# Performance work log

Measured on AMD Instinct MI355X. Metric: run time of the kernel, lower is better.

## Reference

```python
import jax, jax.numpy as jnp
import numpy as np

ATTN_SIZE = 64
ENC_SIZE = 512
HIDDEN_SIZE = 512
L, B = 2048, 64


def setup_inputs() -> dict:
    key = jax.random.key(0)
    k1, k2, k3, k4, k5, k6 = jax.random.split(key, 6)
    enc_outputs = jax.random.normal(k1, (L, B, ENC_SIZE), dtype=jnp.float32)
    lens = jax.random.randint(k2, (B,), 1, L + 1, dtype=jnp.int32)
    hidden_states = jax.random.normal(k3, (B, HIDDEN_SIZE), dtype=jnp.float32)
    # Xavier-normal params as in reset_params()
    W_enc = jax.random.normal(k4, (ENC_SIZE, ATTN_SIZE), dtype=jnp.float32) * np.sqrt(2.0 / (ENC_SIZE + ATTN_SIZE))
    W_hidden = jax.random.normal(k5, (HIDDEN_SIZE, ATTN_SIZE), dtype=jnp.float32) * np.sqrt(2.0 / (HIDDEN_SIZE + ATTN_SIZE))
    b_attn = jnp.zeros((ATTN_SIZE,), dtype=jnp.float32)
    v = jax.random.normal(k6, (ATTN_SIZE,), dtype=jnp.float32)
    return {"enc_outputs": enc_outputs, "lens": lens, "hidden_states": hidden_states,
            "W_enc": W_enc, "b_attn": b_attn, "W_hidden": W_hidden, "v": v}


def reference(enc_outputs, lens, hidden_states, W_enc, b_attn, W_hidden, v):
    l = enc_outputs.shape[0]
    # parts: (l, b, attn_size) — projection of encoder outputs
    parts = jnp.einsum('lbd,da->lba', enc_outputs, W_enc) + b_attn
    # additive (Bahdanau) score: tanh(parts + h @ W_hidden) . v -> (l, b)
    hid = hidden_states @ W_hidden  # (b, attn_size)
    scores = jnp.sum(jnp.tanh(parts + hid[None, :, :]) * v, axis=2)
    # faithful mask: 1.0 at valid positions, -inf at padding (original adds 1, a
    # constant shift that softmax cancels, but we reproduce the exact math)
    valid = jnp.arange(l, dtype=lens.dtype)[:, None] < lens[None, :]  # (l, b)
    mask = jnp.where(valid, jnp.float32(1.0), -jnp.inf)
    w = jax.nn.softmax(scores + mask, axis=0)  # softmax over sequence dim
    # weighted sum over sequence: (b, d)
    return jnp.einsum('lb,lbd->bd', w, enc_outputs)
```

## Files before the change

kernel.cpp:

```cpp
#include <hip/hip_runtime.h>
#include <math.h>

#define L_DIM 2048
#define B_DIM 64
#define D_DIM 512
#define A_DIM 64

__global__ void hb_kernel(const float* __restrict__ hidden,
                          const float* __restrict__ Wh,
                          const float* __restrict__ battn,
                          float* __restrict__ hb) {
    const int b = blockIdx.x;
    const int a = threadIdx.x;
    const float* hrow = hidden + b * D_DIM;
    float acc = battn[a];
#pragma unroll 8
    for (int d = 0; d < D_DIM; ++d) {
        acc += hrow[d] * Wh[d * A_DIM + a];
    }
    hb[b * A_DIM + a] = acc;
}

__global__ __launch_bounds__(256) void scores_kernel(
    const float* __restrict__ enc, const float* __restrict__ We,
    const float* __restrict__ hb, const float* __restrict__ v,
    const int* __restrict__ lens, float* __restrict__ scores) {
    const int l = blockIdx.x;
    const int tid = threadIdx.x;
    const int ty = tid >> 4;
    const int tx = tid & 15;

    __shared__ float As[32][68];
    __shared__ float Bs[32][68];
    __shared__ float red[64][17];

    float acc[4][4] = {};

    float4 areg[2], breg[2];

    const float* encl = enc + (size_t)l * B_DIM * D_DIM;

    auto loadTiles = [&](int k0) {
#pragma unroll
        for (int i = 0; i < 2; ++i) {
            const int c = tid + 256 * i;
            const int bb = c >> 3, kq = c & 7;
            areg[i] = *(const float4*)(encl + bb * D_DIM + k0 + kq * 4);
            const int kk = c >> 4, a4 = (c & 15) * 4;
            breg[i] = *(const float4*)(We + (k0 + kk) * A_DIM + a4);
        }
    };
    auto storeTiles = [&]() {
#pragma unroll
        for (int i = 0; i < 2; ++i) {
            const int c = tid + 256 * i;
            const int bb = c >> 3, kq = c & 7;
            As[kq * 4 + 0][bb] = areg[i].x;
            As[kq * 4 + 1][bb] = areg[i].y;
            As[kq * 4 + 2][bb] = areg[i].z;
            As[kq * 4 + 3][bb] = areg[i].w;
            const int kk = c >> 4, a4 = (c & 15) * 4;
            *(float4*)&Bs[kk][a4] = breg[i];
        }
    };

    loadTiles(0);
#pragma unroll 1
    for (int t = 0; t < 16; ++t) {
        __syncthreads();
        storeTiles();
        __syncthreads();
        if (t < 15) loadTiles((t + 1) * 32);
#pragma unroll
        for (int k = 0; k < 32; ++k) {
            const float4 av = *(const float4*)&As[k][ty * 4];
            const float4 bv = *(const float4*)&Bs[k][tx * 4];
            acc[0][0] += av.x * bv.x; acc[0][1] += av.x * bv.y;
            acc[0][2] += av.x * bv.z; acc[0][3] += av.x * bv.w;
            acc[1][0] += av.y * bv.x; acc[1][1] += av.y * bv.y;
            acc[1][2] += av.y * bv.z; acc[1][3] += av.y * bv.w;
            acc[2][0] += av.z * bv.x; acc[2][1] += av.z * bv.y;
            acc[2][2] += av.z * bv.z; acc[2][3] += av.z * bv.w;
            acc[3][0] += av.w * bv.x; acc[3][1] += av.w * bv.y;
            acc[3][2] += av.w * bv.z; acc[3][3] += av.w * bv.w;
        }
    }

    const float4 vv = *(const float4*)(v + tx * 4);
#pragma unroll
    for (int i = 0; i < 4; ++i) {
        const int bb = ty * 4 + i;
        const float4 hbv = *(const float4*)(hb + bb * A_DIM + tx * 4);
        float s = tanhf(acc[i][0] + hbv.x) * vv.x;
        s += tanhf(acc[i][1] + hbv.y) * vv.y;
        s += tanhf(acc[i][2] + hbv.z) * vv.z;
        s += tanhf(acc[i][3] + hbv.w) * vv.w;
        red[bb][tx] = s;
    }
    __syncthreads();
    if (tid < B_DIM) {
        const int bb = tid;
        float s = 0.f;
#pragma unroll
        for (int j = 0; j < 16; ++j) s += red[bb][j];
        s = (l < lens[bb]) ? (s + 1.0f) : -INFINITY;
        scores[(size_t)bb * L_DIM + l] = s;
    }
}

__global__ __launch_bounds__(256) void softmax_kernel(float* __restrict__ scores) {
    const int b = blockIdx.x;
    const int tid = threadIdx.x;
    float* s = scores + (size_t)b * L_DIM;
    __shared__ float red[256];

    float m = -INFINITY;
    for (int l = tid; l < L_DIM; l += 256) m = fmaxf(m, s[l]);
    red[tid] = m;
    __syncthreads();
    for (int off = 128; off > 0; off >>= 1) {
        if (tid < off) red[tid] = fmaxf(red[tid], red[tid + off]);
        __syncthreads();
    }
    m = red[0];
    __syncthreads();

    float z = 0.f;
    for (int l = tid; l < L_DIM; l += 256) z += expf(s[l] - m);
    red[tid] = z;
    __syncthreads();
    for (int off = 128; off > 0; off >>= 1) {
        if (tid < off) red[tid] += red[tid + off];
        __syncthreads();
    }
    const float inv = 1.0f / red[0];

    for (int l = tid; l < L_DIM; l += 256) s[l] = expf(s[l] - m) * inv;
}

__global__ __launch_bounds__(256) void zero_out_kernel(float* __restrict__ out) {
    out[blockIdx.x * 256 + threadIdx.x] = 0.f;
}

__global__ __launch_bounds__(128) void wsum_kernel(
    const float* __restrict__ enc, const float* __restrict__ w,
    float* __restrict__ out) {
    const int b = blockIdx.x;
    const int lc = blockIdx.y;
    const int tid = threadIdx.x;
    const int l0 = lc * (L_DIM / 16);

    float4 acc = {0.f, 0.f, 0.f, 0.f};
#pragma unroll 4
    for (int l = l0; l < l0 + (L_DIM / 16); ++l) {
        const float wt = w[(size_t)b * L_DIM + l];
        const float4 e =
            *(const float4*)(enc + ((size_t)l * B_DIM + b) * D_DIM + tid * 4);
        acc.x += wt * e.x; acc.y += wt * e.y;
        acc.z += wt * e.z; acc.w += wt * e.w;
    }
    float* o = out + (size_t)b * D_DIM + tid * 4;
    atomicAdd(o + 0, acc.x);
    atomicAdd(o + 1, acc.y);
    atomicAdd(o + 2, acc.z);
    atomicAdd(o + 3, acc.w);
}

extern "C" void kernel_launch(void* const* d_in, const int* in_sizes, int n_in,
                              void* d_out, int out_size, void* d_ws, size_t ws_size,
                              hipStream_t stream) {
    const float* enc    = (const float*)d_in[0];
    const int*   lens   = (const int*)d_in[1];
    const float* hidden = (const float*)d_in[2];
    const float* We     = (const float*)d_in[3];
    const float* battn  = (const float*)d_in[4];
    const float* Wh     = (const float*)d_in[5];
    const float* v      = (const float*)d_in[6];
    float* out = (float*)d_out;

    float* hb     = (float*)d_ws;
    float* scores = hb + B_DIM * A_DIM;

    hb_kernel<<<B_DIM, A_DIM, 0, stream>>>(hidden, Wh, battn, hb);
    scores_kernel<<<L_DIM, 256, 0, stream>>>(enc, We, hb, v, lens, scores);
    softmax_kernel<<<B_DIM, 256, 0, stream>>>(scores);
    zero_out_kernel<<<(B_DIM * D_DIM) / 256, 256, 0, stream>>>(out);
    wsum_kernel<<<dim3(B_DIM, 16), 128, 0, stream>>>(enc, scores, out);
}
```

Baseline: 516.1 us.

## Fuse scores, online softmax and weighted sum with split-bf16 MFMA

Adds a fused kernel that processes 64-position chunks per batch element. Each chunk of encoder data is loaded once, split into bf16 hi/lo parts in shared memory, and projected with bf16 MFMA using three products to keep near-fp32 accuracy. The kernel then computes a chunk-local online softmax and accumulates the weighted sum from the same staged data. A combine kernel merges the per-chunk partials. This removes the second full read of the encoder tensor, the separate softmax pass and the atomics. It costs extra MFMA work and conversion, and it only runs when the workspace is large enough; otherwise the old path is used.

New measurement: 509.1 us. About the same (-1.4%).

```diff
diff --git a/kernel.cpp b/kernel.cpp
--- a/kernel.cpp
+++ b/kernel.cpp
@@ -1,10 +1,31 @@
 #include <hip/hip_runtime.h>
+#include <hip/hip_bf16.h>
 #include <math.h>
 
 #define L_DIM 2048
 #define B_DIM 64
 #define D_DIM 512
 #define A_DIM 64
+
+#define CHUNK_L 64
+#define SUB_L 32
+#define N_CHUNK (L_DIM / CHUNK_L)
+#define EPAD 520
+
+typedef __attribute__((ext_vector_type(8))) short bf16x8;
+typedef __attribute__((ext_vector_type(4))) float f32x4;
+
+__device__ __forceinline__ void split_bf16(float x, short& hi, short& lo) {
+    __hip_bfloat16 h = __float2bfloat16(x);
+    float hf = __bfloat162float(h);
+    __hip_bfloat16 l = __float2bfloat16(x - hf);
+    hi = *reinterpret_cast<short*>(&h);
+    lo = *reinterpret_cast<short*>(&l);
+}
+__device__ __forceinline__ float bf16s_to_f(short s) {
+    unsigned int u = ((unsigned int)(unsigned short)s) << 16;
+    return __uint_as_float(u);
+}
 
 __global__ void hb_kernel(const float* __restrict__ hidden,
                           const float* __restrict__ Wh,
@@ -15,10 +36,231 @@
     const float* hrow = hidden + b * D_DIM;
     float acc = battn[a];
 #pragma unroll 8
-    for (int d = 0; d < D_DIM; ++d) {
-        acc += hrow[d] * Wh[d * A_DIM + a];
-    }
+    for (int d = 0; d < D_DIM; ++d) acc += hrow[d] * Wh[d * A_DIM + a];
     hb[b * A_DIM + a] = acc;
+}
+
+__global__ __launch_bounds__(256) void wt_kernel(const float* __restrict__ We,
+                                                 short* __restrict__ wt_hi,
+                                                 short* __restrict__ wt_lo) {
+    const int idx = blockIdx.x * 256 + threadIdx.x;
+    const int a = idx & 63;
+    const int d = idx >> 6;
+    float x = We[d * A_DIM + a];
+    short h, l;
+    split_bf16(x, h, l);
+    wt_hi[a * D_DIM + d] = h;
+    wt_lo[a * D_DIM + d] = l;
+}
+
+__global__ __launch_bounds__(256) void fused_kernel(
+    const float* __restrict__ enc, const short* __restrict__ wt_hi,
+    const short* __restrict__ wt_lo, const float* __restrict__ hb,
+    const float* __restrict__ v, const int* __restrict__ lens,
+    float* __restrict__ Om, float* __restrict__ mz) {
+    const int c = blockIdx.x;
+    const int b = blockIdx.y;
+    const int tid = threadIdx.x;
+    const int wave = tid >> 6;
+    const int lane = tid & 63;
+    const int quad = lane >> 4;
+    const int l15 = lane & 15;
+
+    __shared__ short Ehi[SUB_L][EPAD];
+    __shared__ short Elo[SUB_L][EPAD];
+    __shared__ float sred[SUB_L][2];
+    __shared__ float wl[SUB_L];
+    __shared__ float red[4][D_DIM];
+    __shared__ float msc[2];
+
+    const int len_b = lens[b];
+
+    const int lt = wave >> 1;
+    const int ah = wave & 1;
+    const int a0 = (2 * ah) * 16 + l15;
+    const int a1 = a0 + 16;
+
+    const float hb0 = hb[b * A_DIM + a0];
+    const float hb1 = hb[b * A_DIM + a1];
+    const float v0 = v[a0];
+    const float v1 = v[a1];
+
+    float Oacc[8];
+#pragma unroll
+    for (int i = 0; i < 8; ++i) Oacc[i] = 0.f;
+    float mA = -INFINITY, ZA = 0.f;
+
+    const int g = tid >> 6;
+    const int d0 = (tid & 63) * 8;
+
+#pragma unroll 1
+    for (int sub = 0; sub < 2; ++sub) {
+        const int l_base = c * CHUNK_L + sub * SUB_L;
+
+        __syncthreads();
+
+        {
+            const float* src = enc + ((size_t)l_base * B_DIM + b) * D_DIM;
+#pragma unroll
+            for (int j = 0; j < 16; ++j) {
+                const int idx = tid + 256 * j;
+                const int li = idx >> 7;
+                const int po = idx & 127;
+                const float4 x =
+                    *(const float4*)(src + (size_t)li * B_DIM * D_DIM + po * 4);
+                short4 h4, l4;
+                split_bf16(x.x, h4.x, l4.x);
+                split_bf16(x.y, h4.y, l4.y);
+                split_bf16(x.z, h4.z, l4.z);
+                split_bf16(x.w, h4.w, l4.w);
+                *(short4*)&Ehi[li][po * 4] = h4;
+                *(short4*)&Elo[li][po * 4] = l4;
+            }
+        }
+        __syncthreads();
+
+        f32x4 acc0 = {0.f, 0.f, 0.f, 0.f};
+        f32x4 acc1 = {0.f, 0.f, 0.f, 0.f};
+        const short* brow0h = wt_hi + (size_t)a0 * D_DIM + quad * 8;
+        const short* brow0l = wt_lo + (size_t)a0 * D_DIM + quad * 8;
+        const short* brow1h = wt_hi + (size_t)a1 * D_DIM + quad * 8;
+        const short* brow1l = wt_lo + (size_t)a1 * D_DIM + quad * 8;
+        const int arow = lt * 16 + l15;
+#pragma unroll 4
+        for (int s = 0; s < 16; ++s) {
+            const int k = s * 32;
+            const bf16x8 Ah = *(const bf16x8*)&Ehi[arow][k + quad * 8];
+            const bf16x8 Al = *(const bf16x8*)&Elo[arow][k + quad * 8];
+            const bf16x8 B0h = *(const bf16x8*)(brow0h + k);
+            const bf16x8 B0l = *(const bf16x8*)(brow0l + k);
+            const bf16x8 B1h = *(const bf16x8*)(brow1h + k);
+            const bf16x8 B1l = *(const bf16x8*)(brow1l + k);
+            acc0 = __builtin_amdgcn_mfma_f32_16x16x32_bf16(Ah, B0h, acc0, 0, 0, 0);
+            acc0 = __builtin_amdgcn_mfma_f32_16x16x32_bf16(Ah, B0l, acc0, 0, 0, 0);
+            acc0 = __builtin_amdgcn_mfma_f32_16x16x32_bf16(Al, B0h, acc0, 0, 0, 0);
+            acc1 = __builtin_amdgcn_mfma_f32_16x16x32_bf16(Ah, B1h, acc1, 0, 0, 0);
+            acc1 = __builtin_amdgcn_mfma_f32_16x16x32_bf16(Ah, B1l, acc1, 0, 0, 0);
+            acc1 = __builtin_amdgcn_mfma_f32_16x16x32_bf16(Al, B1h, acc1, 0, 0, 0);
+        }
+
+#pragma unroll
+        for (int r = 0; r < 4; ++r) {
+            float t = tanhf(acc0[r] + hb0) * v0 + tanhf(acc1[r] + hb1) * v1;
+            t += __shfl_xor(t, 1);
+            t += __shfl_xor(t, 2);
+            t += __shfl_xor(t, 4);
+            t += __shfl_xor(t, 8);
+            if (l15 == 0) sred[lt * 16 + quad * 4 + r][ah] = t;
+        }
+        __syncthreads();
+
+        if (tid < 32) {
+            const int lg = l_base + tid;
+            float s = sred[tid][0] + sred[tid][1];
+            s = (lg < len_b) ? (s + 1.0f) : -INFINITY;
+            float m = s;
+            m = fmaxf(m, __shfl_xor(m, 1));
+            m = fmaxf(m, __shfl_xor(m, 2));
+            m = fmaxf(m, __shfl_xor(m, 4));
+            m = fmaxf(m, __shfl_xor(m, 8));
+            m = fmaxf(m, __shfl_xor(m, 16));
+            const float w = (m == -INFINITY) ? 0.f : expf(s - m);
+            wl[tid] = w;
+            float z = w;
+            z += __shfl_xor(z, 1);
+            z += __shfl_xor(z, 2);
+            z += __shfl_xor(z, 4);
+            z += __shfl_xor(z, 8);
+            z += __shfl_xor(z, 16);
+            if (tid == 0) { msc[0] = m; msc[1] = z; }
+        }
+        __syncthreads();
+
+        float pa[8];
+#pragma unroll
+        for (int i = 0; i < 8; ++i) pa[i] = 0.f;
+#pragma unroll
+        for (int li = 0; li < 8; ++li) {
+            const int l = g * 8 + li;
+            const float w = wl[l];
+            const bf16x8 h8 = *(const bf16x8*)&Ehi[l][d0];
+            const bf16x8 l8 = *(const bf16x8*)&Elo[l][d0];
+#pragma unroll
+            for (int i = 0; i < 8; ++i) {
+                pa[i] += w * (bf16s_to_f(h8[i]) + bf16s_to_f(l8[i]));
+            }
+        }
+        *(float4*)&red[g][d0] = make_float4(pa[0], pa[1], pa[2], pa[3]);
+        *(float4*)&red[g][d0 + 4] = make_float4(pa[4], pa[5], pa[6], pa[7]);
+        __syncthreads();
+
+        const float m_sub = msc[0], Z_sub = msc[1];
+        const float mN = fmaxf(mA, m_sub);
+        const float cA = (mA == -INFINITY) ? 0.f : expf(mA - mN);
+        const float cS = (m_sub == -INFINITY) ? 0.f : expf(m_sub - mN);
+        if (tid < 64) {
+            const int dd = tid * 8;
+#pragma unroll
+            for (int i = 0; i < 8; ++i) {
+                const float os =
+                    red[0][dd + i] + red[1][dd + i] + red[2][dd + i] + red[3][dd + i];
+                Oacc[i] = cA * Oacc[i] + cS * os;
+            }
+        }
+        ZA = cA * ZA + cS * Z_sub;
+        mA = mN;
+    }
+
+    if (tid < 64) {
+        float* dst = Om + ((size_t)b * N_CHUNK + c) * D_DIM + tid * 8;
+        *(float4*)dst = make_float4(Oacc[0], Oacc[1], Oacc[2], Oacc[3]);
+        *(float4*)(dst + 4) = make_float4(Oacc[4], Oacc[5], Oacc[6], Oacc[7]);
+    }
+    if (tid == 0) {
+        mz[((size_t)b * N_CHUNK + c) * 2 + 0] = mA;
+        mz[((size_t)b * N_CHUNK + c) * 2 + 1] = ZA;
+    }
+}
+
+__global__ __launch_bounds__(256) void combine_kernel(
+    const float* __restrict__ Om, const float* __restrict__ mz,
+    float* __restrict__ out) {
+    const int b = blockIdx.x;
+    const int tid = threadIdx.x;
+    __shared__ float coef[N_CHUNK];
+    __shared__ float sinv;
+
+    if (tid < 32) {
+        const float m = mz[((size_t)b * N_CHUNK + tid) * 2 + 0];
+        const float Z = mz[((size_t)b * N_CHUNK + tid) * 2 + 1];
+        float mm = m;
+        mm = fmaxf(mm, __shfl_xor(mm, 1));
+        mm = fmaxf(mm, __shfl_xor(mm, 2));
+        mm = fmaxf(mm, __shfl_xor(mm, 4));
+        mm = fmaxf(mm, __shfl_xor(mm, 8));
+        mm = fmaxf(mm, __shfl_xor(mm, 16));
+        const float cc = (m == -INFINITY) ? 0.f : expf(m - mm);
+        coef[tid] = cc;
+        float s = cc * Z;
+        s += __shfl_xor(s, 1);
+        s += __shfl_xor(s, 2);
+        s += __shfl_xor(s, 4);
+        s += __shfl_xor(s, 8);
+        s += __shfl_xor(s, 16);
+        if (tid == 0) sinv = 1.0f / s;
+    }
+    __syncthreads();
+
+    const float* base = Om + (size_t)b * N_CHUNK * D_DIM + tid * 2;
+    float ox = 0.f, oy = 0.f;
+#pragma unroll 8
+    for (int cc = 0; cc < N_CHUNK; ++cc) {
+        const float2 x = *(const float2*)(base + cc * D_DIM);
+        ox += coef[cc] * x.x;
+        oy += coef[cc] * x.y;
+    }
+    const float s = sinv;
+    *(float2*)(out + (size_t)b * D_DIM + tid * 2) = make_float2(ox * s, oy * s);
 }
 
 __global__ __launch_bounds__(256) void scores_kernel(
@@ -32,34 +274,32 @@
 
     __shared__ float As[32][68];
     __shared__ float Bs[32][68];
-    __shared__ float red[64][17];
+    __shared__ float redl[64][17];
 
     float acc[4][4] = {};
-
     float4 areg[2], breg[2];
-
     const float* encl = enc + (size_t)l * B_DIM * D_DIM;
 
     auto loadTiles = [&](int k0) {
 #pragma unroll
         for (int i = 0; i < 2; ++i) {
-            const int c = tid + 256 * i;
-            const int bb = c >> 3, kq = c & 7;
+            const int cc = tid + 256 * i;
+            const int bb = cc >> 3, kq = cc & 7;
             areg[i] = *(const float4*)(encl + bb * D_DIM + k0 + kq * 4);
-            const int kk = c >> 4, a4 = (c & 15) * 4;
+            const int kk = cc >> 4, a4 = (cc & 15) * 4;
             breg[i] = *(const float4*)(We + (k0 + kk) * A_DIM + a4);
         }
     };
     auto storeTiles = [&]() {
 #pragma unroll
         for (int i = 0; i < 2; ++i) {
-            const int c = tid + 256 * i;
-            const int bb = c >> 3, kq = c & 7;
+            const int cc = tid + 256 * i;
+            const int bb = cc >> 3, kq = cc & 7;
             As[kq * 4 + 0][bb] = areg[i].x;
             As[kq * 4 + 1][bb] = areg[i].y;
             As[kq * 4 + 2][bb] = areg[i].z;
             As[kq * 4 + 3][bb] = areg[i].w;
-            const int kk = c >> 4, a4 = (c & 15) * 4;
+            const int kk = cc >> 4, a4 = (cc & 15) * 4;
             *(float4*)&Bs[kk][a4] = breg[i];
         }
     };
@@ -95,14 +335,14 @@
         s += tanhf(acc[i][1] + hbv.y) * vv.y;
         s += tanhf(acc[i][2] + hbv.z) * vv.z;
         s += tanhf(acc[i][3] + hbv.w) * vv.w;
-        red[bb][tx] = s;
+        redl[bb][tx] = s;
     }
     __syncthreads();
     if (tid < B_DIM) {
         const int bb = tid;
         float s = 0.f;
 #pragma unroll
-        for (int j = 0; j < 16; ++j) s += red[bb][j];
+        for (int j = 0; j < 16; ++j) s += redl[bb][j];
         s = (l < lens[bb]) ? (s + 1.0f) : -INFINITY;
         scores[(size_t)bb * L_DIM + l] = s;
     }
@@ -134,7 +374,6 @@
         __syncthreads();
     }
     const float inv = 1.0f / red[0];
-
     for (int l = tid; l < L_DIM; l += 256) s[l] = expf(s[l] - m) * inv;
 }
 
@@ -178,12 +417,29 @@
     const float* v      = (const float*)d_in[6];
     float* out = (float*)d_out;
 
-    float* hb     = (float*)d_ws;
-    float* scores = hb + B_DIM * A_DIM;
-
-    hb_kernel<<<B_DIM, A_DIM, 0, stream>>>(hidden, Wh, battn, hb);
-    scores_kernel<<<L_DIM, 256, 0, stream>>>(enc, We, hb, v, lens, scores);
-    softmax_kernel<<<B_DIM, 256, 0, stream>>>(scores);
-    zero_out_kernel<<<(B_DIM * D_DIM) / 256, 256, 0, stream>>>(out);
-    wsum_kernel<<<dim3(B_DIM, 16), 128, 0, stream>>>(enc, scores, out);
-}
+    const size_t NEED = (size_t)160 * 1024 + (size_t)4 * 1024 * 1024;
+
+    if (ws_size >= NEED) {
+        char* w8 = (char*)d_ws;
+        float* hb    = (float*)(w8 + 0);
+        short* wt_hi = (short*)(w8 + 16 * 1024);
+        short* wt_lo = (short*)(w8 + 80 * 1024);
+        float* mz    = (float*)(w8 + 144 * 1024);
+        float* Om    = (float*)(w8 + 160 * 1024);
+
+        hb_kernel<<<B_DIM, A_DIM, 0, stream>>>(hidden, Wh, battn, hb);
+        wt_kernel<<<(D_DIM * A_DIM) / 256, 256, 0, stream>>>(We, wt_hi, wt_lo);
+        fused_kernel<<<dim3(N_CHUNK, B_DIM), 256, 0, stream>>>(
+            enc, wt_hi, wt_lo, hb, v, lens, Om, mz);
+        combine_kernel<<<B_DIM, 256, 0, stream>>>(Om, mz, out);
+    } else {
+        float* hb     = (float*)d_ws;
+        float* scores = hb + B_DIM * A_DIM;
+
+        hb_kernel<<<B_DIM, A_DIM, 0, stream>>>(hidden, Wh, battn, hb);
+        scores_kernel<<<L_DIM, 256, 0, stream>>>(enc, We, hb, v, lens, scores);
+        softmax_kernel<<<B_DIM, 256, 0, stream>>>(scores);
+        zero_out_kernel<<<(B_DIM * D_DIM) / 256, 256, 0, stream>>>(out);
+        wsum_kernel<<<dim3(B_DIM, 16), 128, 0, stream>>>(enc, scores, out);
+    }
+}
```
